# Kernel tuning notes

Hardware: AMD Instinct MI355X
Metric: run time of the kernel (lower is better)

Reference implementation:

```python
import jax, jax.numpy as jnp
import numpy as np

N_NODES = 40000
N_EDGES = 640000
IN_C = 128
HID = 32
HEADS = 4
OUT_C = 8
NUM_GRAPHS = 64
NEG_SLOPE = 0.2


def setup_inputs() -> dict:
    key = jax.random.key(0)
    ks = jax.random.split(key, 16)
    x = jax.random.normal(ks[0], (N_NODES, IN_C), dtype=jnp.float32)
    edge_index = jax.random.randint(ks[1], (2, N_EDGES), 0, N_NODES, dtype=jnp.int64)
    batch = jnp.sort(jax.random.randint(ks[2], (N_NODES,), 0, NUM_GRAPHS, dtype=jnp.int64))
    s = lambda k, shape, fan_in: jax.random.normal(k, shape, jnp.float32) / np.sqrt(fan_in)
    # conv0: in -> hid, 4 heads, concat
    W0 = s(ks[3], (IN_C, HEADS * HID), IN_C)
    a_src0 = s(ks[4], (HEADS, HID), HID)
    a_dst0 = s(ks[5], (HEADS, HID), HID)
    b0 = jnp.zeros((HEADS * HID,), jnp.float32)
    # conv1: hid*H -> hid, 4 heads, concat
    W1 = s(ks[6], (HEADS * HID, HEADS * HID), HEADS * HID)
    a_src1 = s(ks[7], (HEADS, HID), HID)
    a_dst1 = s(ks[8], (HEADS, HID), HID)
    b1 = jnp.zeros((HEADS * HID,), jnp.float32)
    # conv2: hid*H -> hid, 1 head, no concat
    W2 = s(ks[9], (HEADS * HID, HID), HEADS * HID)
    a_src2 = s(ks[10], (1, HID), HID)
    a_dst2 = s(ks[11], (1, HID), HID)
    b2 = jnp.zeros((HID,), jnp.float32)
    lin1_w = s(ks[12], (HID, IN_C), HID)
    lin1_b = jnp.zeros((IN_C,), jnp.float32)
    lin2_w = s(ks[13], (IN_C, OUT_C), IN_C)
    lin2_b = jnp.zeros((OUT_C,), jnp.float32)
    return dict(x=x, edge_index=edge_index, batch=batch,
                W0=W0, a_src0=a_src0, a_dst0=a_dst0, b0=b0,
                W1=W1, a_src1=a_src1, a_dst1=a_dst1, b1=b1,
                W2=W2, a_src2=a_src2, a_dst2=a_dst2, b2=b2,
                lin1_w=lin1_w, lin1_b=lin1_b, lin2_w=lin2_w, lin2_b=lin2_b)


def gat_conv(x, src, dst, W, a_src, a_dst, b, heads, out_c, concat):
    N = x.shape[0]
    h = (x @ W).reshape(N, heads, out_c)          # [N,H,C]
    als = (h * a_src[None]).sum(-1)               # [N,H]
    ald = (h * a_dst[None]).sum(-1)               # [N,H]
    e = jax.nn.leaky_relu(als[src] + ald[dst], NEG_SLOPE)  # [E,H]
    m = jax.ops.segment_max(e, dst, num_segments=N)
    m = jnp.where(jnp.isfinite(m), m, 0.0)
    p = jnp.exp(e - m[dst])                       # [E,H]
    denom = jax.ops.segment_sum(p, dst, num_segments=N)
    alpha = p / jnp.maximum(denom[dst], 1e-16)
    out = jax.ops.segment_sum(h[src] * alpha[:, :, None], dst, num_segments=N)
    out = out.reshape(N, heads * out_c) if concat else out.mean(axis=1)
    return out + b


def reference(x, edge_index, batch,
              W0, a_src0, a_dst0, b0,
              W1, a_src1, a_dst1, b1,
              W2, a_src2, a_dst2, b2,
              lin1_w, lin1_b, lin2_w, lin2_b):
    N = x.shape[0]
    # PyG GATConv adds self-loops by default
    loop = jnp.arange(N, dtype=edge_index.dtype)
    src = jnp.concatenate([edge_index[0], loop])
    dst = jnp.concatenate([edge_index[1], loop])
    # eval mode: dropout is identity
    h = jax.nn.elu(gat_conv(x, src, dst, W0, a_src0, a_dst0, b0, HEADS, HID, True))
    h = jax.nn.elu(gat_conv(h, src, dst, W1, a_src1, a_dst1, b1, HEADS, HID, True))
    h = jax.nn.elu(gat_conv(h, src, dst, W2, a_src2, a_dst2, b2, 1, HID, False))
    # global mean pool over graphs
    sums = jax.ops.segment_sum(h, batch, num_segments=NUM_GRAPHS)
    cnts = jax.ops.segment_sum(jnp.ones((N, 1), h.dtype), batch, num_segments=NUM_GRAPHS)
    g = sums / jnp.maximum(cnts, 1.0)             # [G, HID]
    g = jax.nn.relu(g @ lin1_w + lin1_b)
    return g @ lin2_w + lin2_b                    # [G, OUT_C]
```

## Files before the change

### kernel.cpp

```cpp
#include <hip/hip_runtime.h>

#define N_NODES 40000
#define N_EDGES 640000
#define E_TOT   (N_EDGES + N_NODES)
#define NUM_GRAPHS 64
#define CAP_SHIFT 6

#define CVTX_BLOCKS 5000
#define CVTW_BLOCKS 144
#define GEMM_BLOCKS 625

#define BINS 157
#define BIN_CAP 5120
#define TBLK 4096
#define A2BLKS ((N_EDGES + TBLK - 1) / TBLK)

typedef __attribute__((ext_vector_type(8))) short bf16x8;
typedef __attribute__((ext_vector_type(4))) float f32x4;

__device__ inline float bf2f(unsigned short u) {
    union { unsigned int i; float f; } v; v.i = ((unsigned int)u) << 16; return v.f;
}
__device__ inline unsigned short f2bf(float f) {
    union { float f; unsigned int i; } v; v.f = f;
    unsigned int r = v.i + 0x7FFF + ((v.i >> 16) & 1);
    return (unsigned short)(r >> 16);
}


__device__ void binA2_body(int ab, const int* __restrict__ esrc,
                           const int* __restrict__ edst,
                           int* __restrict__ bin_gcnt,
                           unsigned int* __restrict__ bins) {
    __shared__ unsigned int ebuf[TBLK];
    __shared__ int bcnt[BINS];
    __shared__ int scn[256];
    __shared__ int lbase[BINS];
    __shared__ int boff[BINS];
    __shared__ int gbase[BINS];
    int tid = threadIdx.x;
    for (int i = tid; i < BINS; i += 256) bcnt[i] = 0;
    __syncthreads();
    int ebase = ab * TBLK;
    int ecount = N_EDGES - ebase; if (ecount > TBLK) ecount = TBLK;
    unsigned int ent[16];
#pragma unroll
    for (int k = 0; k < 16; ++k) {
        int idx = k * 256 + tid;
        ent[k] = 0xFFFFFFFFu;
        if (idx < ecount) {
            int e = ebase + idx;
            int d = edst[e], s = esrc[e];
            ent[k] = ((unsigned int)(d >> 8) << 24) |
                     ((unsigned int)(d & 255) << 16) | (unsigned int)s;
            atomicAdd(&bcnt[d >> 8], 1);
        }
    }
    __syncthreads();
    scn[tid] = (tid < BINS) ? bcnt[tid] : 0;
    __syncthreads();
    for (int off = 1; off < 256; off <<= 1) {
        int u = (tid >= off) ? scn[tid - off] : 0;
        __syncthreads();
        scn[tid] += u;
        __syncthreads();
    }
    if (tid < BINS) {
        lbase[tid] = scn[tid] - bcnt[tid];
        boff[tid] = 0;
        if (bcnt[tid]) gbase[tid] = atomicAdd(&bin_gcnt[tid], bcnt[tid]);
    }
    __syncthreads();
#pragma unroll
    for (int k = 0; k < 16; ++k) {
        unsigned int e = ent[k];
        if (e != 0xFFFFFFFFu) {
            int bin = e >> 24;
            int pos = lbase[bin] + atomicAdd(&boff[bin], 1);
            ebuf[pos] = e;
        }
    }
    __syncthreads();
    for (int i = tid; i < ecount; i += 256) {
        unsigned int e = ebuf[i];
        int bin = e >> 24;
        bins[bin * BIN_CAP + gbase[bin] + (i - lbase[bin])] = e & 0x00FFFFFFu;
    }
}


__global__ __launch_bounds__(256) void cvt_binA_kernel(const float* __restrict__ x,
                                                       const float* __restrict__ W0,
                                                       const float* __restrict__ W1,
                                                       const float* __restrict__ W2,
                                                       unsigned short* __restrict__ Xb,
                                                       unsigned short* __restrict__ Wt0,
                                                       unsigned short* __restrict__ Wt1,
                                                       unsigned short* __restrict__ Wt2,
                                                       const int* __restrict__ esrc,
                                                       const int* __restrict__ edst,
                                                       int* __restrict__ bin_gcnt,
                                                       unsigned int* __restrict__ bins) {
    int b = blockIdx.x;
    int tid = threadIdx.x;
    if (b < A2BLKS) {
        binA2_body(b, esrc, edst, bin_gcnt, bins);
    } else if (b < A2BLKS + CVTX_BLOCKS) {
        int i = (b - A2BLKS) * 256 + tid;
        float4 v = ((const float4*)x)[i];
        ushort4 o;
        o.x = f2bf(v.x); o.y = f2bf(v.y); o.z = f2bf(v.z); o.w = f2bf(v.w);
        ((ushort4*)Xb)[i] = o;
    } else {
        int idx = (b - A2BLKS - CVTX_BLOCKS) * 256 + tid;
        if (idx < 16384) {
            int n = idx >> 7, k = idx & 127;
            Wt0[idx] = f2bf(W0[k * 128 + n]);
        } else if (idx < 32768) {
            int i = idx - 16384;
            int n = i >> 7, k = i & 127;
            Wt1[i] = f2bf(W1[k * 128 + n]);
        } else if (idx < 36864) {
            int i = idx - 32768;
            int n = i >> 7, k = i & 127;
            Wt2[i] = f2bf(W2[k * 32 + n]);
        }
    }
}


__device__ void binB_body(int bb, const int* __restrict__ bin_gcnt,
                          const unsigned int* __restrict__ bins,
                          int* __restrict__ cnt,
                          unsigned short* __restrict__ psrc) {
    __shared__ unsigned short lbuck[256 * 64];
    __shared__ int lcnt[256];
    int tid = threadIdx.x;
    lcnt[tid] = 0;
    __syncthreads();
    int cntE = bin_gcnt[bb];
    for (int i = tid; i < cntE; i += 256) {
        unsigned int entry = bins[bb * BIN_CAP + i];
        int dl = entry >> 16;
        int pos = atomicAdd(&lcnt[dl], 1);
        lbuck[dl * 64 + pos] = (unsigned short)(entry & 0xFFFFu);
    }
    __syncthreads();
    int node = bb * 256 + tid;
    if (node < N_NODES) {
        int pos = lcnt[tid];
        lbuck[tid * 64 + pos] = (unsigned short)node;
        lcnt[tid] = pos + 1;
    }
    __syncthreads();
    int base = bb * (256 * 64);
    int lim = (bb == BINS - 1) ? ((N_NODES - bb * 256) * 64) : (256 * 64);
    for (int i = tid; i < lim; i += 256)
        psrc[base + i] = lbuck[i];
    if (node < N_NODES) cnt[node] = lcnt[tid];
}


__device__ __forceinline__ void gemm128_body(int blk,
                                             const unsigned short* __restrict__ Xb,
                                             const unsigned short* __restrict__ Wt,
                                             const float* __restrict__ asrc,
                                             const float* __restrict__ adst,
                                             unsigned short* __restrict__ Hb,
                                             float* __restrict__ ALS4,
                                             float* __restrict__ ALD4) {
    int wave = threadIdx.x >> 6;
    int lane = threadIdx.x & 63;
    int l15 = lane & 15;
    int q = lane >> 4;
    int r0 = (blk * 4 + wave) * 16;

    f32x4 acc[8];
#pragma unroll
    for (int t = 0; t < 8; ++t) acc[t] = (f32x4){0.f, 0.f, 0.f, 0.f};

    float asv[8], adv[8];
#pragma unroll
    for (int t = 0; t < 8; ++t) {
        int c = t * 16 + l15;
        asv[t] = asrc[c];
        adv[t] = adst[c];
    }

    const unsigned short* xrow = Xb + (long)(r0 + l15) * 128 + q * 8;
    const unsigned short* wrow = Wt + (long)l15 * 128 + q * 8;
#pragma unroll
    for (int kt = 0; kt < 4; ++kt) {
        bf16x8 a = *(const bf16x8*)(xrow + kt * 32);
#pragma unroll
        for (int t = 0; t < 8; ++t) {
            bf16x8 b = *(const bf16x8*)(wrow + (long)t * 16 * 128 + kt * 32);
            acc[t] = __builtin_amdgcn_mfma_f32_16x16x32_bf16(a, b, acc[t], 0, 0, 0);
        }
    }

#pragma unroll
    for (int t = 0; t < 8; ++t)
#pragma unroll
        for (int i = 0; i < 4; ++i)
            Hb[(long)(r0 + q * 4 + i) * 128 + t * 16 + l15] = f2bf(acc[t][i]);

#pragma unroll
    for (int i = 0; i < 4; ++i) {
        float ps0 = acc[0][i] * asv[0] + acc[1][i] * asv[1];
        float ps1 = acc[2][i] * asv[2] + acc[3][i] * asv[3];
        float ps2 = acc[4][i] * asv[4] + acc[5][i] * asv[5];
        float ps3 = acc[6][i] * asv[6] + acc[7][i] * asv[7];
        float pd0 = acc[0][i] * adv[0] + acc[1][i] * adv[1];
        float pd1 = acc[2][i] * adv[2] + acc[3][i] * adv[3];
        float pd2 = acc[4][i] * adv[4] + acc[5][i] * adv[5];
        float pd3 = acc[6][i] * adv[6] + acc[7][i] * adv[7];
#pragma unroll
        for (int m = 1; m < 16; m <<= 1) {
            ps0 += __shfl_xor(ps0, m, 16); ps1 += __shfl_xor(ps1, m, 16);
            ps2 += __shfl_xor(ps2, m, 16); ps3 += __shfl_xor(ps3, m, 16);
            pd0 += __shfl_xor(pd0, m, 16); pd1 += __shfl_xor(pd1, m, 16);
            pd2 += __shfl_xor(pd2, m, 16); pd3 += __shfl_xor(pd3, m, 16);
        }
        int r = r0 + q * 4 + i;
        if (l15 < 4) {
            float v = (l15 == 0) ? ps0 : (l15 == 1) ? ps1 : (l15 == 2) ? ps2 : ps3;
            ALS4[r * 4 + l15] = v;
        } else if (l15 < 8) {
            int h = l15 - 4;
            float v = (h == 0) ? pd0 : (h == 1) ? pd1 : (h == 2) ? pd2 : pd3;
            ALD4[r * 4 + h] = v;
        }
    }
}

__global__ __launch_bounds__(256) void gemm0_binB_kernel(const unsigned short* __restrict__ Xb,
                                                         const unsigned short* __restrict__ Wt,
                                                         const float* __restrict__ asrc,
                                                         const float* __restrict__ adst,
                                                         unsigned short* __restrict__ Hb,
                                                         float* __restrict__ ALS4,
                                                         float* __restrict__ ALD4,
                                                         const int* __restrict__ bin_gcnt,
                                                         const unsigned int* __restrict__ bins,
                                                         int* __restrict__ cnt,
                                                         unsigned short* __restrict__ psrc) {
    int b = blockIdx.x;
    if (b < BINS) {
        binB_body(b, bin_gcnt, bins, cnt, psrc);
    } else {
        gemm128_body(b - BINS, Xb, Wt, asrc, adst, Hb, ALS4, ALD4);
    }
}

__global__ __launch_bounds__(256) void gemm128_mfma(const unsigned short* __restrict__ Xb,
                                                    const unsigned short* __restrict__ Wt,
                                                    const float* __restrict__ asrc,
                                                    const float* __restrict__ adst,
                                                    unsigned short* __restrict__ Hb,
                                                    float* __restrict__ ALS4,
                                                    float* __restrict__ ALD4) {
    gemm128_body(blockIdx.x, Xb, Wt, asrc, adst, Hb, ALS4, ALD4);
}

__global__ __launch_bounds__(256) void gemm32_mfma(const unsigned short* __restrict__ Xb,
                                                   const unsigned short* __restrict__ Wt2,
                                                   const float* __restrict__ asrc,
                                                   const float* __restrict__ adst,
                                                   unsigned short* __restrict__ H2b,
                                                   float* __restrict__ ALS,
                                                   float* __restrict__ ALD) {
    int wave = threadIdx.x >> 6;
    int lane = threadIdx.x & 63;
    int l15 = lane & 15;
    int q = lane >> 4;
    int r0 = (blockIdx.x * 4 + wave) * 16;

    f32x4 acc[2];
    acc[0] = (f32x4){0.f, 0.f, 0.f, 0.f};
    acc[1] = (f32x4){0.f, 0.f, 0.f, 0.f};

    const unsigned short* xrow = Xb + (long)(r0 + l15) * 128 + q * 8;
    const unsigned short* wrow = Wt2 + (long)l15 * 128 + q * 8;
#pragma unroll
    for (int kt = 0; kt < 4; ++kt) {
        bf16x8 a = *(const bf16x8*)(xrow + kt * 32);
#pragma unroll
        for (int t = 0; t < 2; ++t) {
            bf16x8 b = *(const bf16x8*)(wrow + (long)t * 16 * 128 + kt * 32);
            acc[t] = __builtin_amdgcn_mfma_f32_16x16x32_bf16(a, b, acc[t], 0, 0, 0);
        }
    }

    float as0 = asrc[l15], as1 = asrc[16 + l15];
    float ad0 = adst[l15], ad1 = adst[16 + l15];
#pragma unroll
    for (int t = 0; t < 2; ++t)
#pragma unroll
        for (int i = 0; i < 4; ++i)
            H2b[(long)(r0 + q * 4 + i) * 32 + t * 16 + l15] = f2bf(acc[t][i]);

#pragma unroll
    for (int i = 0; i < 4; ++i) {
        float ps = acc[0][i] * as0 + acc[1][i] * as1;
        float pd = acc[0][i] * ad0 + acc[1][i] * ad1;
#pragma unroll
        for (int m = 1; m < 16; m <<= 1) {
            ps += __shfl_xor(ps, m, 16);
            pd += __shfl_xor(pd, m, 16);
        }
        if (l15 == 0) {
            int r = r0 + q * 4 + i;
            ALS[r] = ps;
            ALD[r] = pd;
        }
    }
}

__global__ __launch_bounds__(256) void agg128(const unsigned short* __restrict__ Hb,
                                              const float* __restrict__ ALS4,
                                              const float* __restrict__ ALD4,
                                              const int* __restrict__ cnt,
                                              const unsigned short* __restrict__ psrc,
                                              const float* __restrict__ bias,
                                              unsigned short* __restrict__ OUTb) {
    int n = blockIdx.x * 4 + (threadIdx.x >> 6);
    n = __builtin_amdgcn_readfirstlane(n);
    if (n >= N_NODES) return;
    int lane = threadIdx.x & 63;
    int c = lane * 2;
    int head = lane >> 4;
    int e16 = lane & 15;
    float aldh = ALD4[n * 4 + head];
    int j0 = n << CAP_SHIFT;
    int j1 = j0 + __builtin_amdgcn_readfirstlane(cnt[n]);
    float a0 = 0.f, a1 = 0.f, dsum = 0.f;
    for (int jb = j0; jb < j1; jb += 16) {
        int j = jb + e16;
        int jc = (j < j1) ? j : (j1 - 1);
        int s = (int)psrc[jc];
        float e = ALS4[s * 4 + head] + aldh;
        e = (e > 0.f) ? e : 0.2f * e;
        float w = (j < j1) ? __expf(e) : 0.f;
        int st[16]; float wt[16];
#pragma unroll
        for (int t = 0; t < 16; ++t) {
            st[t] = __shfl(s, t, 16);
            wt[t] = __shfl(w, t, 16);
        }
        unsigned int hv[16];
#pragma unroll
        for (int t = 0; t < 16; ++t)
            hv[t] = *(const unsigned int*)(Hb + (long)st[t] * 128 + c);
#pragma unroll
        for (int t = 0; t < 16; ++t) {
            float h0 = bf2f((unsigned short)(hv[t] & 0xFFFF));
            float h1 = bf2f((unsigned short)(hv[t] >> 16));
            dsum += wt[t];
            a0 += wt[t] * h0;
            a1 += wt[t] * h1;
        }
    }
    float inv = 1.0f / dsum;
    float o0 = a0 * inv + bias[c];
    float o1 = a1 * inv + bias[c + 1];
    o0 = (o0 > 0.f) ? o0 : (__expf(o0) - 1.f);
    o1 = (o1 > 0.f) ? o1 : (__expf(o1) - 1.f);
    ushort2 ob; ob.x = f2bf(o0); ob.y = f2bf(o1);
    *(ushort2*)(OUTb + (long)n * 128 + c) = ob;
}

__global__ __launch_bounds__(256) void agg32(const unsigned short* __restrict__ H2b,
                                             const float* __restrict__ ALS,
                                             const float* __restrict__ ALD,
                                             const int* __restrict__ cnt,
                                             const unsigned short* __restrict__ psrc,
                                             const float* __restrict__ bias,
                                             float* __restrict__ OUT) {
    int wv = blockIdx.x * 4 + (threadIdx.x >> 6);
    int lane = threadIdx.x & 63;
    int col = lane & 31;
    int half = lane >> 5;
    int e16 = lane & 15;
    int n = wv * 2 + half;
    if (n >= N_NODES) return;
    float aldn = ALD[n];
    int j0 = n << CAP_SHIFT;
    int j1 = j0 + cnt[n];
    float a = 0.f, dsum = 0.f;
    for (int jb = j0; jb < j1; jb += 16) {
        int j = jb + e16;
        int jc = (j < j1) ? j : (j1 - 1);
        int s = (int)psrc[jc];
        float e = ALS[s] + aldn;
        e = (e > 0.f) ? e : 0.2f * e;
        float w = (j < j1) ? __expf(e) : 0.f;
        int st[16]; float wt[16];
#pragma unroll
        for (int t = 0; t < 16; ++t) {
            st[t] = __shfl(s, t, 16);
            wt[t] = __shfl(w, t, 16);
        }
        unsigned short hv[16];
#pragma unroll
        for (int t = 0; t < 16; ++t)
            hv[t] = H2b[st[t] * 32 + col];
#pragma unroll
        for (int t = 0; t < 16; ++t) {
            dsum += wt[t];
            a += wt[t] * bf2f(hv[t]);
        }
    }
    float o = a / dsum + bias[col];
    o = (o > 0.f) ? o : (__expf(o) - 1.f);
    OUT[n * 32 + col] = o;
}

__global__ __launch_bounds__(256) void pool_kernel(const float* __restrict__ H3,
                                                   const int* __restrict__ batch,
                                                   float* __restrict__ gsum,
                                                   float* __restrict__ gcnt) {
    const int CHUNK = 40;
    int gid = (blockIdx.x * 256 + threadIdx.x) >> 5;
    int c = threadIdx.x & 31;
    int n0 = gid * CHUNK;
    if (n0 >= N_NODES) return;
    int n1 = n0 + CHUNK;
    if (n1 > N_NODES) n1 = N_NODES;
    int cur = batch[n0];
    float acc = 0.f;
    int cnt = 0;
    for (int n = n0; n < n1; ++n) {
        int b = batch[n];
        if (b != cur) {
            atomicAdd(&gsum[cur * 32 + c], acc);
            if (c == 0) atomicAdd(&gcnt[cur], (float)cnt);
            cur = b; acc = 0.f; cnt = 0;
        }
        acc += H3[n * 32 + c];
        cnt++;
    }
    atomicAdd(&gsum[cur * 32 + c], acc);
    if (c == 0) atomicAdd(&gcnt[cur], (float)cnt);
}

__global__ __launch_bounds__(256) void mlp_kernel(const float* __restrict__ gsum,
                                                  const float* __restrict__ gcnt,
                                                  const float* __restrict__ l1w,
                                                  const float* __restrict__ l1b,
                                                  const float* __restrict__ l2w,
                                                  const float* __restrict__ l2b,
                                                  float* __restrict__ out) {
    __shared__ float g[NUM_GRAPHS * 32];
    __shared__ float t1[NUM_GRAPHS * 128];
    int tid = threadIdx.x;
    for (int i = tid; i < NUM_GRAPHS * 32; i += 256) {
        float c = gcnt[i >> 5];
        g[i] = gsum[i] / fmaxf(c, 1.0f);
    }
    __syncthreads();
    for (int i = tid; i < NUM_GRAPHS * 128; i += 256) {
        int r = i >> 7, j = i & 127;
        float a = l1b[j];
        for (int k = 0; k < 32; ++k) a += g[r * 32 + k] * l1w[k * 128 + j];
        t1[i] = fmaxf(a, 0.f);
    }
    __syncthreads();
    for (int i = tid; i < NUM_GRAPHS * 8; i += 256) {
        int r = i >> 3, j = i & 7;
        float a = l2b[j];
        for (int k = 0; k < 128; ++k) a += t1[r * 128 + k] * l2w[k * 8 + j];
        out[i] = a;
    }
}


extern "C" void kernel_launch(void* const* d_in, const int* in_sizes, int n_in,
                              void* d_out, int out_size, void* d_ws, size_t ws_size,
                              hipStream_t stream) {
    const float* x      = (const float*)d_in[0];
    const int*   eidx   = (const int*)d_in[1];
    const int*   batch  = (const int*)d_in[2];
    const float* W0     = (const float*)d_in[3];
    const float* asrc0  = (const float*)d_in[4];
    const float* adst0  = (const float*)d_in[5];
    const float* b0     = (const float*)d_in[6];
    const float* W1     = (const float*)d_in[7];
    const float* asrc1  = (const float*)d_in[8];
    const float* adst1  = (const float*)d_in[9];
    const float* b1     = (const float*)d_in[10];
    const float* W2     = (const float*)d_in[11];
    const float* asrc2  = (const float*)d_in[12];
    const float* adst2  = (const float*)d_in[13];
    const float* b2     = (const float*)d_in[14];
    const float* l1w    = (const float*)d_in[15];
    const float* l1b    = (const float*)d_in[16];
    const float* l2w    = (const float*)d_in[17];
    const float* l2b    = (const float*)d_in[18];
    float* out = (float*)d_out;

    const int* esrc = eidx;
    const int* edst = eidx + N_EDGES;

    float* ALS  = (float*)d_ws;
    float* ALD  = ALS + N_NODES * 4;
    float* h3   = ALD + N_NODES * 4;
    int* cnt    = (int*)(h3 + (long)N_NODES * 32);
    int* bin_gcnt = cnt + N_NODES;
    float* gsum = (float*)(bin_gcnt + BINS);
    float* gcnt = gsum + NUM_GRAPHS * 32;
    unsigned int* bins = (unsigned int*)(gcnt + NUM_GRAPHS);
    unsigned short* psrc = (unsigned short*)(bins + (long)BINS * BIN_CAP);
    uintptr_t p = (uintptr_t)(psrc + ((long)N_NODES << CAP_SHIFT));
    p = (p + 15) & ~(uintptr_t)15;
    unsigned short* Xb   = (unsigned short*)p;
    unsigned short* Hb   = Xb + (long)N_NODES * 128;
    unsigned short* OUTb = Hb + (long)N_NODES * 128;
    unsigned short* H2b  = OUTb + (long)N_NODES * 128;
    unsigned short* Wt0  = H2b + (long)N_NODES * 32;
    unsigned short* Wt1  = Wt0 + 128 * 128;
    unsigned short* Wt2  = Wt1 + 128 * 128;

    size_t zbytes = (size_t)(BINS + NUM_GRAPHS * 32 + NUM_GRAPHS) * 4;
    hipMemsetAsync(bin_gcnt, 0, zbytes, stream);

    cvt_binA_kernel<<<A2BLKS + CVTX_BLOCKS + CVTW_BLOCKS, 256, 0, stream>>>(
        x, W0, W1, W2, Xb, Wt0, Wt1, Wt2, esrc, edst, bin_gcnt, bins);

    gemm0_binB_kernel<<<BINS + GEMM_BLOCKS, 256, 0, stream>>>(
        Xb, Wt0, asrc0, adst0, Hb, ALS, ALD, bin_gcnt, bins, cnt, psrc);
    agg128<<<10000, 256, 0, stream>>>(Hb, ALS, ALD, cnt, psrc, b0, OUTb);

    gemm128_mfma<<<GEMM_BLOCKS, 256, 0, stream>>>(OUTb, Wt1, asrc1, adst1, Hb, ALS, ALD);
    agg128<<<10000, 256, 0, stream>>>(Hb, ALS, ALD, cnt, psrc, b1, OUTb);

    gemm32_mfma<<<GEMM_BLOCKS, 256, 0, stream>>>(OUTb, Wt2, asrc2, adst2, H2b, ALS, ALD);
    agg32<<<5000, 256, 0, stream>>>(H2b, ALS, ALD, cnt, psrc, b2, h3);

    pool_kernel<<<125, 256, 0, stream>>>(h3, batch, gsum, gcnt);
    mlp_kernel<<<1, 256, 0, stream>>>(gsum, gcnt, l1w, l1b, l2w, l2b, out);
}
```

Measured before the change: 272.0 us.

## Use 16-byte row loads in agg128 and reduce edge partials across lane groups

Restructures the 128-channel GAT aggregation so each lane loads 8 bf16 channels (16 bytes) from a source row. Each of the four 16-lane groups handles a different quarter of the edges in every 16-edge batch, and the partial sums are combined at the end with xor shuffles. This replaces sixteen 4-byte gathers per lane per batch with four 16-byte gathers, aiming to cut memory instruction count and improve gather efficiency. The cost is a cross-group shuffle reduction and only one quarter of the lanes writing output.

```diff
diff --git a/kernel.cpp b/kernel.cpp
--- a/kernel.cpp
+++ b/kernel.cpp
@@ -17,6 +17,7 @@
 
 typedef __attribute__((ext_vector_type(8))) short bf16x8;
 typedef __attribute__((ext_vector_type(4))) float f32x4;
+typedef __attribute__((ext_vector_type(8))) unsigned short u16x8;
 
 __device__ inline float bf2f(unsigned short u) {
     union { unsigned int i; float f; } v; v.i = ((unsigned int)u) << 16; return v.f;
@@ -328,46 +329,67 @@
     n = __builtin_amdgcn_readfirstlane(n);
     if (n >= N_NODES) return;
     int lane = threadIdx.x & 63;
-    int c = lane * 2;
-    int head = lane >> 4;
-    int e16 = lane & 15;
-    float aldh = ALD4[n * 4 + head];
+    int sub = lane & 15;
+    int q = lane >> 4;
+    int hh = sub >> 2;
+    float aldh = ALD4[n * 4 + q];
     int j0 = n << CAP_SHIFT;
     int j1 = j0 + __builtin_amdgcn_readfirstlane(cnt[n]);
-    float a0 = 0.f, a1 = 0.f, dsum = 0.f;
+    f32x4 a0 = (f32x4){0.f, 0.f, 0.f, 0.f};
+    f32x4 a1 = (f32x4){0.f, 0.f, 0.f, 0.f};
+    float dsum = 0.f;
+    int wb = hh * 16 + q;
     for (int jb = j0; jb < j1; jb += 16) {
-        int j = jb + e16;
+        int j = jb + sub;
         int jc = (j < j1) ? j : (j1 - 1);
         int s = (int)psrc[jc];
-        float e = ALS4[s * 4 + head] + aldh;
+        float e = ALS4[s * 4 + q] + aldh;
         e = (e > 0.f) ? e : 0.2f * e;
         float w = (j < j1) ? __expf(e) : 0.f;
-        int st[16]; float wt[16];
-#pragma unroll
-        for (int t = 0; t < 16; ++t) {
-            st[t] = __shfl(s, t, 16);
-            wt[t] = __shfl(w, t, 16);
-        }
-        unsigned int hv[16];
-#pragma unroll
-        for (int t = 0; t < 16; ++t)
-            hv[t] = *(const unsigned int*)(Hb + (long)st[t] * 128 + c);
-#pragma unroll
-        for (int t = 0; t < 16; ++t) {
-            float h0 = bf2f((unsigned short)(hv[t] & 0xFFFF));
-            float h1 = bf2f((unsigned short)(hv[t] >> 16));
-            dsum += wt[t];
-            a0 += wt[t] * h0;
-            a1 += wt[t] * h1;
-        }
-    }
-    float inv = 1.0f / dsum;
-    float o0 = a0 * inv + bias[c];
-    float o1 = a1 * inv + bias[c + 1];
-    o0 = (o0 > 0.f) ? o0 : (__expf(o0) - 1.f);
-    o1 = (o1 > 0.f) ? o1 : (__expf(o1) - 1.f);
-    ushort2 ob; ob.x = f2bf(o0); ob.y = f2bf(o1);
-    *(ushort2*)(OUTb + (long)n * 128 + c) = ob;
+        int st0 = __shfl(s, q, 16);
+        int st1 = __shfl(s, 4 + q, 16);
+        int st2 = __shfl(s, 8 + q, 16);
+        int st3 = __shfl(s, 12 + q, 16);
+        u16x8 h0 = *(const u16x8*)(Hb + (long)st0 * 128 + sub * 8);
+        u16x8 h1 = *(const u16x8*)(Hb + (long)st1 * 128 + sub * 8);
+        u16x8 h2 = *(const u16x8*)(Hb + (long)st2 * 128 + sub * 8);
+        u16x8 h3 = *(const u16x8*)(Hb + (long)st3 * 128 + sub * 8);
+        float w0 = __shfl(w, wb, 64);
+        float w1 = __shfl(w, wb + 4, 64);
+        float w2 = __shfl(w, wb + 8, 64);
+        float w3 = __shfl(w, wb + 12, 64);
+        dsum += (w0 + w1) + (w2 + w3);
+#pragma unroll
+        for (int k = 0; k < 4; ++k) {
+            a0[k] += w0 * bf2f(h0[k]) + w1 * bf2f(h1[k])
+                   + w2 * bf2f(h2[k]) + w3 * bf2f(h3[k]);
+            a1[k] += w0 * bf2f(h0[k + 4]) + w1 * bf2f(h1[k + 4])
+                   + w2 * bf2f(h2[k + 4]) + w3 * bf2f(h3[k + 4]);
+        }
+    }
+#pragma unroll
+    for (int m = 16; m <= 32; m <<= 1) {
+        dsum += __shfl_xor(dsum, m, 64);
+#pragma unroll
+        for (int k = 0; k < 4; ++k) {
+            a0[k] += __shfl_xor(a0[k], m, 64);
+            a1[k] += __shfl_xor(a1[k], m, 64);
+        }
+    }
+    if (q == 0) {
+        float inv = 1.0f / dsum;
+        u16x8 ob;
+#pragma unroll
+        for (int k = 0; k < 4; ++k) {
+            float o = a0[k] * inv + bias[sub * 8 + k];
+            o = (o > 0.f) ? o : (__expf(o) - 1.f);
+            ob[k] = f2bf(o);
+            float o2 = a1[k] * inv + bias[sub * 8 + 4 + k];
+            o2 = (o2 > 0.f) ? o2 : (__expf(o2) - 1.f);
+            ob[k + 4] = f2bf(o2);
+        }
+        *(u16x8*)(OUTb + (long)n * 128 + sub * 8) = ob;
+    }
 }
 
 __global__ __launch_bounds__(256) void agg32(const unsigned short* __restrict__ H2b,
```

Result: no change. 272.4 us (+0.2%).

## Fuse attention aggregation with the next layer's GEMM through an LDS tile

Applied to the files above, without the earlier changes.

Each layer's edge aggregation (softmax-weighted gather, bias, ELU) is merged with the next layer's MFMA projection. Each block aggregates 64 nodes into a swizzled shared-memory tile, then multiplies that tile by the next weight matrix. This removes the global write and re-read of the intermediate activations and two kernel launches. Ping-pong buffers are added for H and the attention logits so a layer does not overwrite its own inputs. The cost is fewer blocks (625 instead of 10000), so there is less parallelism for the latency-bound gather phase and more load imbalance within a block.

```diff
diff --git a/kernel.cpp b/kernel.cpp
--- a/kernel.cpp
+++ b/kernel.cpp
@@ -253,53 +253,209 @@
     }
 }
 
-__global__ __launch_bounds__(256) void gemm128_mfma(const unsigned short* __restrict__ Xb,
-                                                    const unsigned short* __restrict__ Wt,
-                                                    const float* __restrict__ asrc,
-                                                    const float* __restrict__ adst,
-                                                    unsigned short* __restrict__ Hb,
-                                                    float* __restrict__ ALS4,
-                                                    float* __restrict__ ALD4) {
-    gemm128_body(blockIdx.x, Xb, Wt, asrc, adst, Hb, ALS4, ALD4);
-}
-
-__global__ __launch_bounds__(256) void gemm32_mfma(const unsigned short* __restrict__ Xb,
-                                                   const unsigned short* __restrict__ Wt2,
+__global__ __launch_bounds__(256) void agg_gemm128(const unsigned short* __restrict__ HbIn,
+                                                   const float* __restrict__ ALS4i,
+                                                   const float* __restrict__ ALD4i,
+                                                   const int* __restrict__ cnt,
+                                                   const unsigned short* __restrict__ psrc,
+                                                   const float* __restrict__ bias,
+                                                   const unsigned short* __restrict__ Wt,
                                                    const float* __restrict__ asrc,
                                                    const float* __restrict__ adst,
-                                                   unsigned short* __restrict__ H2b,
-                                                   float* __restrict__ ALS,
-                                                   float* __restrict__ ALD) {
-    int wave = threadIdx.x >> 6;
+                                                   unsigned short* __restrict__ HbOut,
+                                                   float* __restrict__ ALS4o,
+                                                   float* __restrict__ ALD4o) {
+    __shared__ unsigned short tile[64 * 128];
+    int wv = threadIdx.x >> 6;
     int lane = threadIdx.x & 63;
+    int nbase = blockIdx.x * 64;
+    int c = lane * 2;
+    int head = lane >> 4;
+    int e16 = lane & 15;
+    for (int it = 0; it < 16; ++it) {
+        int n = __builtin_amdgcn_readfirstlane(nbase + it * 4 + wv);
+        float aldh = ALD4i[n * 4 + head];
+        int j0 = n << CAP_SHIFT;
+        int j1 = j0 + __builtin_amdgcn_readfirstlane(cnt[n]);
+        float a0 = 0.f, a1 = 0.f, dsum = 0.f;
+        for (int jb = j0; jb < j1; jb += 16) {
+            int j = jb + e16;
+            int jc = (j < j1) ? j : (j1 - 1);
+            int s = (int)psrc[jc];
+            float e = ALS4i[s * 4 + head] + aldh;
+            e = (e > 0.f) ? e : 0.2f * e;
+            float w = (j < j1) ? __expf(e) : 0.f;
+            int st[16]; float wt[16];
+#pragma unroll
+            for (int t = 0; t < 16; ++t) {
+                st[t] = __shfl(s, t, 16);
+                wt[t] = __shfl(w, t, 16);
+            }
+            unsigned int hv[16];
+#pragma unroll
+            for (int t = 0; t < 16; ++t)
+                hv[t] = *(const unsigned int*)(HbIn + (long)st[t] * 128 + c);
+#pragma unroll
+            for (int t = 0; t < 16; ++t) {
+                dsum += wt[t];
+                a0 += wt[t] * bf2f((unsigned short)(hv[t] & 0xFFFF));
+                a1 += wt[t] * bf2f((unsigned short)(hv[t] >> 16));
+            }
+        }
+        float inv = 1.0f / dsum;
+        float o0 = a0 * inv + bias[c];
+        float o1 = a1 * inv + bias[c + 1];
+        o0 = (o0 > 0.f) ? o0 : (__expf(o0) - 1.f);
+        o1 = (o1 > 0.f) ? o1 : (__expf(o1) - 1.f);
+        int row = it * 4 + wv;
+        int col = c ^ ((row & 7) << 3);
+        ushort2 ob; ob.x = f2bf(o0); ob.y = f2bf(o1);
+        *(ushort2*)&tile[row * 128 + col] = ob;
+    }
+    __syncthreads();
     int l15 = lane & 15;
     int q = lane >> 4;
-    int r0 = (blockIdx.x * 4 + wave) * 16;
-
+    f32x4 acc[8];
+#pragma unroll
+    for (int t = 0; t < 8; ++t) acc[t] = (f32x4){0.f, 0.f, 0.f, 0.f};
+    float asv[8], adv[8];
+#pragma unroll
+    for (int t = 0; t < 8; ++t) {
+        asv[t] = asrc[t * 16 + l15];
+        adv[t] = adst[t * 16 + l15];
+    }
+    int row = wv * 16 + l15;
+    const unsigned short* wrow = Wt + (long)l15 * 128 + q * 8;
+#pragma unroll
+    for (int kt = 0; kt < 4; ++kt) {
+        int e0 = (q * 8 + kt * 32) ^ ((row & 7) << 3);
+        bf16x8 a = *(const bf16x8*)&tile[row * 128 + e0];
+#pragma unroll
+        for (int t = 0; t < 8; ++t) {
+            bf16x8 b = *(const bf16x8*)(wrow + (long)t * 16 * 128 + kt * 32);
+            acc[t] = __builtin_amdgcn_mfma_f32_16x16x32_bf16(a, b, acc[t], 0, 0, 0);
+        }
+    }
+    int r0 = nbase + wv * 16;
+#pragma unroll
+    for (int t = 0; t < 8; ++t)
+#pragma unroll
+        for (int i = 0; i < 4; ++i)
+            HbOut[(long)(r0 + q * 4 + i) * 128 + t * 16 + l15] = f2bf(acc[t][i]);
+#pragma unroll
+    for (int i = 0; i < 4; ++i) {
+        float ps0 = acc[0][i] * asv[0] + acc[1][i] * asv[1];
+        float ps1 = acc[2][i] * asv[2] + acc[3][i] * asv[3];
+        float ps2 = acc[4][i] * asv[4] + acc[5][i] * asv[5];
+        float ps3 = acc[6][i] * asv[6] + acc[7][i] * asv[7];
+        float pd0 = acc[0][i] * adv[0] + acc[1][i] * adv[1];
+        float pd1 = acc[2][i] * adv[2] + acc[3][i] * adv[3];
+        float pd2 = acc[4][i] * adv[4] + acc[5][i] * adv[5];
+        float pd3 = acc[6][i] * adv[6] + acc[7][i] * adv[7];
+#pragma unroll
+        for (int m = 1; m < 16; m <<= 1) {
+            ps0 += __shfl_xor(ps0, m, 16); ps1 += __shfl_xor(ps1, m, 16);
+            ps2 += __shfl_xor(ps2, m, 16); ps3 += __shfl_xor(ps3, m, 16);
+            pd0 += __shfl_xor(pd0, m, 16); pd1 += __shfl_xor(pd1, m, 16);
+            pd2 += __shfl_xor(pd2, m, 16); pd3 += __shfl_xor(pd3, m, 16);
+        }
+        int r = r0 + q * 4 + i;
+        if (l15 < 4) {
+            float v = (l15 == 0) ? ps0 : (l15 == 1) ? ps1 : (l15 == 2) ? ps2 : ps3;
+            ALS4o[r * 4 + l15] = v;
+        } else if (l15 < 8) {
+            int h = l15 - 4;
+            float v = (h == 0) ? pd0 : (h == 1) ? pd1 : (h == 2) ? pd2 : pd3;
+            ALD4o[r * 4 + h] = v;
+        }
+    }
+}
+
+__global__ __launch_bounds__(256) void agg_gemm32(const unsigned short* __restrict__ HbIn,
+                                                  const float* __restrict__ ALS4i,
+                                                  const float* __restrict__ ALD4i,
+                                                  const int* __restrict__ cnt,
+                                                  const unsigned short* __restrict__ psrc,
+                                                  const float* __restrict__ bias,
+                                                  const unsigned short* __restrict__ Wt2,
+                                                  const float* __restrict__ asrc,
+                                                  const float* __restrict__ adst,
+                                                  unsigned short* __restrict__ H2b,
+                                                  float* __restrict__ ALS,
+                                                  float* __restrict__ ALD) {
+    __shared__ unsigned short tile[64 * 128];
+    int wv = threadIdx.x >> 6;
+    int lane = threadIdx.x & 63;
+    int nbase = blockIdx.x * 64;
+    int c = lane * 2;
+    int head = lane >> 4;
+    int e16 = lane & 15;
+    for (int it = 0; it < 16; ++it) {
+        int n = __builtin_amdgcn_readfirstlane(nbase + it * 4 + wv);
+        float aldh = ALD4i[n * 4 + head];
+        int j0 = n << CAP_SHIFT;
+        int j1 = j0 + __builtin_amdgcn_readfirstlane(cnt[n]);
+        float a0 = 0.f, a1 = 0.f, dsum = 0.f;
+        for (int jb = j0; jb < j1; jb += 16) {
+            int j = jb + e16;
+            int jc = (j < j1) ? j : (j1 - 1);
+            int s = (int)psrc[jc];
+            float e = ALS4i[s * 4 + head] + aldh;
+            e = (e > 0.f) ? e : 0.2f * e;
+            float w = (j < j1) ? __expf(e) : 0.f;
+            int st[16]; float wt[16];
+#pragma unroll
+            for (int t = 0; t < 16; ++t) {
+                st[t] = __shfl(s, t, 16);
+                wt[t] = __shfl(w, t, 16);
+            }
+            unsigned int hv[16];
+#pragma unroll
+            for (int t = 0; t < 16; ++t)
+                hv[t] = *(const unsigned int*)(HbIn + (long)st[t] * 128 + c);
+#pragma unroll
+            for (int t = 0; t < 16; ++t) {
+                dsum += wt[t];
+                a0 += wt[t] * bf2f((unsigned short)(hv[t] & 0xFFFF));
+                a1 += wt[t] * bf2f((unsigned short)(hv[t] >> 16));
+            }
+        }
+        float inv = 1.0f / dsum;
+        float o0 = a0 * inv + bias[c];
+        float o1 = a1 * inv + bias[c + 1];
+        o0 = (o0 > 0.f) ? o0 : (__expf(o0) - 1.f);
+        o1 = (o1 > 0.f) ? o1 : (__expf(o1) - 1.f);
+        int row = it * 4 + wv;
+        int col = c ^ ((row & 7) << 3);
+        ushort2 ob; ob.x = f2bf(o0); ob.y = f2bf(o1);
+        *(ushort2*)&tile[row * 128 + col] = ob;
+    }
+    __syncthreads();
+    int l15 = lane & 15;
+    int q = lane >> 4;
     f32x4 acc[2];
     acc[0] = (f32x4){0.f, 0.f, 0.f, 0.f};
     acc[1] = (f32x4){0.f, 0.f, 0.f, 0.f};
-
-    const unsigned short* xrow = Xb + (long)(r0 + l15) * 128 + q * 8;
+    int row = wv * 16 + l15;
     const unsigned short* wrow = Wt2 + (long)l15 * 128 + q * 8;
 #pragma unroll
     for (int kt = 0; kt < 4; ++kt) {
-        bf16x8 a = *(const bf16x8*)(xrow + kt * 32);
+        int e0 = (q * 8 + kt * 32) ^ ((row & 7) << 3);
+        bf16x8 a = *(const bf16x8*)&tile[row * 128 + e0];
 #pragma unroll
         for (int t = 0; t < 2; ++t) {
             bf16x8 b = *(const bf16x8*)(wrow + (long)t * 16 * 128 + kt * 32);
             acc[t] = __builtin_amdgcn_mfma_f32_16x16x32_bf16(a, b, acc[t], 0, 0, 0);
         }
     }
-
     float as0 = asrc[l15], as1 = asrc[16 + l15];
     float ad0 = adst[l15], ad1 = adst[16 + l15];
+    int r0 = nbase + wv * 16;
 #pragma unroll
     for (int t = 0; t < 2; ++t)
 #pragma unroll
         for (int i = 0; i < 4; ++i)
             H2b[(long)(r0 + q * 4 + i) * 32 + t * 16 + l15] = f2bf(acc[t][i]);
-
 #pragma unroll
     for (int i = 0; i < 4; ++i) {
         float ps = acc[0][i] * as0 + acc[1][i] * as1;
@@ -315,59 +471,6 @@
             ALD[r] = pd;
         }
     }
-}
-
-__global__ __launch_bounds__(256) void agg128(const unsigned short* __restrict__ Hb,
-                                              const float* __restrict__ ALS4,
-                                              const float* __restrict__ ALD4,
-                                              const int* __restrict__ cnt,
-                                              const unsigned short* __restrict__ psrc,
-                                              const float* __restrict__ bias,
-                                              unsigned short* __restrict__ OUTb) {
-    int n = blockIdx.x * 4 + (threadIdx.x >> 6);
-    n = __builtin_amdgcn_readfirstlane(n);
-    if (n >= N_NODES) return;
-    int lane = threadIdx.x & 63;
-    int c = lane * 2;
-    int head = lane >> 4;
-    int e16 = lane & 15;
-    float aldh = ALD4[n * 4 + head];
-    int j0 = n << CAP_SHIFT;
-    int j1 = j0 + __builtin_amdgcn_readfirstlane(cnt[n]);
-    float a0 = 0.f, a1 = 0.f, dsum = 0.f;
-    for (int jb = j0; jb < j1; jb += 16) {
-        int j = jb + e16;
-        int jc = (j < j1) ? j : (j1 - 1);
-        int s = (int)psrc[jc];
-        float e = ALS4[s * 4 + head] + aldh;
-        e = (e > 0.f) ? e : 0.2f * e;
-        float w = (j < j1) ? __expf(e) : 0.f;
-        int st[16]; float wt[16];
-#pragma unroll
-        for (int t = 0; t < 16; ++t) {
-            st[t] = __shfl(s, t, 16);
-            wt[t] = __shfl(w, t, 16);
-        }
-        unsigned int hv[16];
-#pragma unroll
-        for (int t = 0; t < 16; ++t)
-            hv[t] = *(const unsigned int*)(Hb + (long)st[t] * 128 + c);
-#pragma unroll
-        for (int t = 0; t < 16; ++t) {
-            float h0 = bf2f((unsigned short)(hv[t] & 0xFFFF));
-            float h1 = bf2f((unsigned short)(hv[t] >> 16));
-            dsum += wt[t];
-            a0 += wt[t] * h0;
-            a1 += wt[t] * h1;
-        }
-    }
-    float inv = 1.0f / dsum;
-    float o0 = a0 * inv + bias[c];
-    float o1 = a1 * inv + bias[c + 1];
-    o0 = (o0 > 0.f) ? o0 : (__expf(o0) - 1.f);
-    o1 = (o1 > 0.f) ? o1 : (__expf(o1) - 1.f);
-    ushort2 ob; ob.x = f2bf(o0); ob.y = f2bf(o1);
-    *(ushort2*)(OUTb + (long)n * 128 + c) = ob;
 }
 
 __global__ __launch_bounds__(256) void agg32(const unsigned short* __restrict__ H2b,
@@ -502,9 +605,13 @@
     const int* esrc = eidx;
     const int* edst = eidx + N_EDGES;
 
-    float* ALS  = (float*)d_ws;
-    float* ALD  = ALS + N_NODES * 4;
-    float* h3   = ALD + N_NODES * 4;
+    float* ALS0 = (float*)d_ws;
+    float* ALD0 = ALS0 + N_NODES * 4;
+    float* ALS1 = ALD0 + N_NODES * 4;
+    float* ALD1 = ALS1 + N_NODES * 4;
+    float* ALS2 = ALD1 + N_NODES * 4;
+    float* ALD2 = ALS2 + N_NODES;
+    float* h3   = ALD2 + N_NODES;
     int* cnt    = (int*)(h3 + (long)N_NODES * 32);
     int* bin_gcnt = cnt + N_NODES;
     float* gsum = (float*)(bin_gcnt + BINS);
@@ -514,9 +621,9 @@
     uintptr_t p = (uintptr_t)(psrc + ((long)N_NODES << CAP_SHIFT));
     p = (p + 15) & ~(uintptr_t)15;
     unsigned short* Xb   = (unsigned short*)p;
-    unsigned short* Hb   = Xb + (long)N_NODES * 128;
-    unsigned short* OUTb = Hb + (long)N_NODES * 128;
-    unsigned short* H2b  = OUTb + (long)N_NODES * 128;
+    unsigned short* Hb0  = Xb + (long)N_NODES * 128;
+    unsigned short* Hb1  = Hb0 + (long)N_NODES * 128;
+    unsigned short* H2b  = Hb1 + (long)N_NODES * 128;
     unsigned short* Wt0  = H2b + (long)N_NODES * 32;
     unsigned short* Wt1  = Wt0 + 128 * 128;
     unsigned short* Wt2  = Wt1 + 128 * 128;
@@ -528,14 +635,15 @@
         x, W0, W1, W2, Xb, Wt0, Wt1, Wt2, esrc, edst, bin_gcnt, bins);
 
     gemm0_binB_kernel<<<BINS + GEMM_BLOCKS, 256, 0, stream>>>(
-        Xb, Wt0, asrc0, adst0, Hb, ALS, ALD, bin_gcnt, bins, cnt, psrc);
-    agg128<<<10000, 256, 0, stream>>>(Hb, ALS, ALD, cnt, psrc, b0, OUTb);
-
-    gemm128_mfma<<<GEMM_BLOCKS, 256, 0, stream>>>(OUTb, Wt1, asrc1, adst1, Hb, ALS, ALD);
-    agg128<<<10000, 256, 0, stream>>>(Hb, ALS, ALD, cnt, psrc, b1, OUTb);
-
-    gemm32_mfma<<<GEMM_BLOCKS, 256, 0, stream>>>(OUTb, Wt2, asrc2, adst2, H2b, ALS, ALD);
-    agg32<<<5000, 256, 0, stream>>>(H2b, ALS, ALD, cnt, psrc, b2, h3);
+        Xb, Wt0, asrc0, adst0, Hb0, ALS0, ALD0, bin_gcnt, bins, cnt, psrc);
+
+    agg_gemm128<<<GEMM_BLOCKS, 256, 0, stream>>>(
+        Hb0, ALS0, ALD0, cnt, psrc, b0, Wt1, asrc1, adst1, Hb1, ALS1, ALD1);
+
+    agg_gemm32<<<GEMM_BLOCKS, 256, 0, stream>>>(
+        Hb1, ALS1, ALD1, cnt, psrc, b1, Wt2, asrc2, adst2, H2b, ALS2, ALD2);
+
+    agg32<<<5000, 256, 0, stream>>>(H2b, ALS2, ALD2, cnt, psrc, b2, h3);
 
     pool_kernel<<<125, 256, 0, stream>>>(h3, batch, gsum, gcnt);
     mlp_kernel<<<1, 256, 0, stream>>>(gsum, gcnt, l1w, l1b, l2w, l2b, out);
```

New measurement: 286.0 us. 1.05x slower.
